# Kernel optimization log

Measured on AMD Instinct MI355X. Metric: run time of the kernel, lower is better.

## Reference

```python
import jax, jax.numpy as jnp
import numpy as np
from jax import lax

B, N, G, K, D = 16, 8192, 256, 64, 256
DEPTH, H, HID, PH = 4, 8, 1024, 128
EPS = 1e-5
BN_SCALE = float(1.0 / np.sqrt(1.0 + 1e-5))  # BatchNorm eval, running mean 0 / var 1


def setup_inputs() -> dict:
    key = jax.random.key(0)
    ks = iter(jax.random.split(key, 48))
    def rn(shape, s=0.02):
        return jax.random.normal(next(ks), shape, jnp.float32) * s
    z = lambda *s: jnp.zeros(s, jnp.float32)
    o = lambda *s: jnp.ones(s, jnp.float32)
    return dict(
        x=jax.random.normal(next(ks), (B, N, 3), jnp.float32),
        enc_w1=rn((3, 128)), enc_b1=z(128), enc_bn1_g=o(128), enc_bn1_b=z(128),
        enc_w2=rn((128, 256)), enc_b2=z(256),
        enc_w3=rn((512, 512)), enc_b3=z(512), enc_bn2_g=o(512), enc_bn2_b=z(512),
        enc_w4=rn((512, D)), enc_b4=z(D),
        cls_token=rn((1, 1, D)), cls_pos=rn((1, 1, D)),
        pos_w1=rn((3, 128)), pos_b1=z(128), pos_w2=rn((128, D)), pos_b2=z(D),
        ln1_g=o(DEPTH, D), ln1_b=z(DEPTH, D),
        qkv_w=rn((DEPTH, D, 3 * D)),
        proj_w=rn((DEPTH, D, D)), proj_b=z(DEPTH, D),
        ln2_g=o(DEPTH, D), ln2_b=z(DEPTH, D),
        fc1_w=rn((DEPTH, D, HID)), fc1_b=z(DEPTH, HID),
        fc2_w=rn((DEPTH, HID, D)), fc2_b=z(DEPTH, D),
        norm_g=o(D), norm_b=z(D),
        head_w1=rn((D + 3, PH)), head_b1=z(PH), head_w2=rn((PH, 1)), head_b2=z(1),
    )


def layernorm(t, g, b):
    m = jnp.mean(t, -1, keepdims=True)
    v = jnp.mean((t - m) ** 2, -1, keepdims=True)
    return (t - m) / jnp.sqrt(v + EPS) * g + b


def fps(xyz, num_group):
    # farthest point sampling; deterministic start at index 0 (torch uses randint)
    Bb, Nn, _ = xyz.shape
    def body(i, st):
        dist, far, idxs = st
        idxs = idxs.at[:, i].set(far)
        cen = jnp.take_along_axis(xyz, far[:, None, None], axis=1)  # (B,1,3)
        d = jnp.sum((xyz - cen) ** 2, -1)
        dist = jnp.minimum(dist, d)
        far = jnp.argmax(dist, axis=1).astype(jnp.int32)
        return (dist, far, idxs)
    st0 = (jnp.full((Bb, Nn), 1e10, jnp.float32),
           jnp.zeros((Bb,), jnp.int32),
           jnp.zeros((Bb, num_group), jnp.int32))
    _, _, idxs = lax.fori_loop(0, num_group, body, st0)
    centers = jnp.take_along_axis(xyz, idxs[..., None], axis=1)  # (B,G,3)
    return centers, idxs


def knn(xyz, centers, k):
    # squared-distance cdist (same argsort order as p=2) + topk smallest
    c2 = jnp.sum(centers ** 2, -1)[:, :, None]
    x2 = jnp.sum(xyz ** 2, -1)[:, None, :]
    d2 = c2 + x2 - 2.0 * jnp.einsum('bgd,bnd->bgn', centers, xyz)  # (B,G,N)
    idx = lax.top_k(-d2, k)[1]  # (B,G,k)
    neigh = jax.vmap(lambda p, i: p[i])(xyz, idx)  # (B,G,k,3)
    return idx, neigh


def _forward(x, enc_w1, enc_b1, enc_bn1_g, enc_bn1_b, enc_w2, enc_b2,
             enc_w3, enc_b3, enc_bn2_g, enc_bn2_b, enc_w4, enc_b4,
             cls_token, cls_pos, pos_w1, pos_b1, pos_w2, pos_b2,
             ln1_g, ln1_b, qkv_w, proj_w, proj_b, ln2_g, ln2_b,
             fc1_w, fc1_b, fc2_w, fc2_b, norm_g, norm_b,
             head_w1, head_b1, head_w2, head_b2):
    Bb, Nn, _ = x.shape
    # grouping is @torch.no_grad() in the original -> stop_gradient
    pts = lax.stop_gradient(x)
    centers, _ = fps(pts, G)
    idx, neigh = knn(pts, centers, K)
    neigh = neigh - centers[:, :, None, :]  # (B,G,K,3) centered

    # PointNet encoder (kernel-size-1 convs == matmuls; BN eval with unit stats)
    pg = neigh.reshape(Bb * G, K, 3)
    h = pg @ enc_w1 + enc_b1                                # (BG,K,128)
    h = jax.nn.relu(h * enc_bn1_g * BN_SCALE + enc_bn1_b)
    h = h @ enc_w2 + enc_b2                                 # (BG,K,256)
    gmax = jnp.max(h, axis=1, keepdims=True)                # (BG,1,256)
    h = jnp.concatenate([jnp.broadcast_to(gmax, h.shape), h], -1)  # (BG,K,512)
    h = h @ enc_w3 + enc_b3
    h = jax.nn.relu(h * enc_bn2_g * BN_SCALE + enc_bn2_b)
    h = h @ enc_w4 + enc_b4                                 # (BG,K,D)
    tokens = jnp.max(h, axis=1).reshape(Bb, G, D)

    pos = jax.nn.gelu(centers @ pos_w1 + pos_b1, approximate=False) @ pos_w2 + pos_b2
    xt = jnp.concatenate([jnp.broadcast_to(cls_token, (Bb, 1, D)), tokens], 1)
    pt = jnp.concatenate([jnp.broadcast_to(cls_pos, (Bb, 1, D)), pos], 1)

    scale = (D // H) ** -0.5
    for l in range(DEPTH):
        xi = xt + pt  # pos added before every block
        h1 = layernorm(xi, ln1_g[l], ln1_b[l])
        qkv = (h1 @ qkv_w[l]).reshape(Bb, G + 1, 3, H, D // H).transpose(2, 0, 3, 1, 4)
        q, k_, v = qkv[0], qkv[1], qkv[2]
        attn = jax.nn.softmax(jnp.einsum('bhnd,bhmd->bhnm', q, k_) * scale, -1)
        o = jnp.einsum('bhnm,bhmd->bhnd', attn, v).transpose(0, 2, 1, 3).reshape(Bb, G + 1, D)
        xi = xi + o @ proj_w[l] + proj_b[l]
        h2 = layernorm(xi, ln2_g[l], ln2_b[l])
        xi = xi + jax.nn.gelu(h2 @ fc1_w[l] + fc1_b[l], approximate=False) @ fc2_w[l] + fc2_b[l]
        xt = xi
    xt = layernorm(xt, norm_g, norm_b)

    gfeat = xt[:, 1:, :]  # (B,G,D)
    concat = jnp.concatenate(
        [jnp.broadcast_to(gfeat[:, :, None, :], (Bb, G, K, D)), neigh], -1)  # (B,G,K,D+3)
    lg = (jax.nn.relu(concat @ head_w1 + head_b1) @ head_w2 + head_b2)[..., 0]  # (B,G,K)

    # scatter-mean per-point logits over original N points
    flat_i = idx.reshape(Bb, G * K)
    flat_v = lg.reshape(Bb, G * K)
    sums = jax.vmap(lambda v, i: jax.ops.segment_sum(v, i, num_segments=N))(flat_v, flat_i)
    cnts = jax.vmap(lambda i: jax.ops.segment_sum(jnp.ones(i.shape, jnp.float32), i, num_segments=N))(flat_i)
    return sums / jnp.maximum(cnts, 1.0)  # (B,N)


def reference(x, enc_w1, enc_b1, enc_bn1_g, enc_bn1_b, enc_w2, enc_b2,
              enc_w3, enc_b3, enc_bn2_g, enc_bn2_b, enc_w4, enc_b4,
              cls_token, cls_pos, pos_w1, pos_b1, pos_w2, pos_b2,
              ln1_g, ln1_b, qkv_w, proj_w, proj_b, ln2_g, ln2_b,
              fc1_w, fc1_b, fc2_w, fc2_b, norm_g, norm_b,
              head_w1, head_b1, head_w2, head_b2):
    return _forward(x, enc_w1, enc_b1, enc_bn1_g, enc_bn1_b, enc_w2, enc_b2,
                    enc_w3, enc_b3, enc_bn2_g, enc_bn2_b, enc_w4, enc_b4,
                    cls_token, cls_pos, pos_w1, pos_b1, pos_w2, pos_b2,
                    ln1_g, ln1_b, qkv_w, proj_w, proj_b, ln2_g, ln2_b,
                    fc1_w, fc1_b, fc2_w, fc2_b, norm_g, norm_b,
                    head_w1, head_b1, head_w2, head_b2)
```

## Files before the change

kernel.cpp:

```cpp
#include <hip/hip_runtime.h>
#include <hip/hip_bf16.h>

#define B_ 16
#define N_ 8192
#define G_ 256
#define K_ 64
#define D_ 256
#define HID_ 1024
#define EPS_ 1e-5f

typedef __attribute__((ext_vector_type(8))) short bf16x8;
typedef __attribute__((ext_vector_type(4))) float f32x4;

__device__ __forceinline__ float bf16_to_f32(unsigned short u){
  unsigned int v = ((unsigned int)u) << 16;
  return __uint_as_float(v);
}
__device__ __forceinline__ unsigned short f32_to_bf16(float f){
  unsigned int u = __float_as_uint(f);
  unsigned int r = (u + 0x7FFFu + ((u >> 16) & 1u)) >> 16;
  return (unsigned short)r;
}
__device__ __forceinline__ unsigned short bf16h(float a){
  __hip_bfloat16 h = __float2bfloat16(a);
  union { __hip_bfloat16 h; unsigned short u; } cv; cv.h = h; return cv.u;
}
__device__ __forceinline__ float gelu_exact(float v){
  return 0.5f * v * (1.0f + erff(v * 0.70710678118654752440f));
}

template<int CTRL>
__device__ __forceinline__ unsigned long long dpp64(unsigned long long k){
  int lo = (int)(unsigned int)k;
  int hi = (int)(unsigned int)(k >> 32);
  int dlo = __builtin_amdgcn_update_dpp(lo, lo, CTRL, 0xF, 0xF, false);
  int dhi = __builtin_amdgcn_update_dpp(hi, hi, CTRL, 0xF, 0xF, false);
  return (((unsigned long long)(unsigned int)dhi) << 32) | (unsigned int)dlo;
}
__device__ __forceinline__ unsigned long long bcast64(unsigned long long k, int lane){
  unsigned int lo = (unsigned int)__builtin_amdgcn_readlane((int)(unsigned int)k, lane);
  unsigned int hi = (unsigned int)__builtin_amdgcn_readlane((int)(unsigned int)(k >> 32), lane);
  return (((unsigned long long)hi) << 32) | lo;
}
__device__ __forceinline__ unsigned long long wave_max64(unsigned long long k){
  unsigned long long t;
  t = dpp64<0x111>(k); if (t > k) k = t;
  t = dpp64<0x112>(k); if (t > k) k = t;
  t = dpp64<0x114>(k); if (t > k) k = t;
  t = dpp64<0x118>(k); if (t > k) k = t;
  t = dpp64<0x142>(k); if (t > k) k = t;
  t = dpp64<0x143>(k); if (t > k) k = t;
  return bcast64(k, 63);
}
__device__ __forceinline__ unsigned long long wave_min64(unsigned long long k){
  unsigned long long t;
  t = dpp64<0x111>(k); if (t < k) k = t;
  t = dpp64<0x112>(k); if (t < k) k = t;
  t = dpp64<0x114>(k); if (t < k) k = t;
  t = dpp64<0x118>(k); if (t < k) k = t;
  t = dpp64<0x142>(k); if (t < k) k = t;
  t = dpp64<0x143>(k); if (t < k) k = t;
  return bcast64(k, 63);
}
__device__ __forceinline__ unsigned long long red8_max64(unsigned long long k){
  unsigned long long t;
  t = dpp64<0x111>(k); if (t > k) k = t;
  t = dpp64<0x112>(k); if (t > k) k = t;
  t = dpp64<0x114>(k); if (t > k) k = t;
  return bcast64(k, 7);
}
__device__ __forceinline__ unsigned long long red4_min64(unsigned long long k){
  unsigned long long t;
  t = dpp64<0x111>(k); if (t < k) k = t;
  t = dpp64<0x112>(k); if (t < k) k = t;
  return bcast64(k, 3);
}

__device__ __forceinline__ void packHi(const float* __restrict__ W, unsigned short* __restrict__ hi,
                                       int f, int N, int ksBits){
  int j = f & 7, lane = (f >> 3) & 63;
  int ks = (f >> 9) & ((1 << ksBits) - 1);
  int nt = f >> (9 + ksBits);
  int k = ks * 32 + ((lane >> 4) & 3) * 8 + j, c = nt * 16 + (lane & 15);
  hi[f] = f32_to_bf16(W[(size_t)k * N + c]);
}

__global__ __launch_bounds__(512)
__attribute__((amdgpu_waves_per_eu(2, 2)))
void prep_fps_kernel(
    const float* __restrict__ x, float* __restrict__ centers,
    const float* __restrict__ w1, const float* __restrict__ b1,
    const float* __restrict__ g1, const float* __restrict__ bb1,
    const float* __restrict__ w3, const float* __restrict__ b3,
    const float* __restrict__ g2, const float* __restrict__ bb2,
    const float* __restrict__ enc_w2, const float* __restrict__ enc_w4,
    const float* __restrict__ qkv_w, const float* __restrict__ proj_w,
    const float* __restrict__ fc1_w, const float* __restrict__ fc2_w,
    float* __restrict__ w1f, float* __restrict__ b1f, float* __restrict__ b3f,
    unsigned short* __restrict__ w2ph, unsigned short* __restrict__ w2pl,
    unsigned short* __restrict__ w3ph, unsigned short* __restrict__ w4ph,
    unsigned short* __restrict__ qkvPh, unsigned short* __restrict__ projPh,
    unsigned short* __restrict__ fc1Ph, unsigned short* __restrict__ fc2Ph,
    unsigned short* __restrict__ w3tp)
{
  const float S = 0.99999500003749968f;
  int blk = blockIdx.x, tid = threadIdx.x;

  if (blk >= 17){
    int f = (blk - 17) * 512 + tid;
    if (f < 32768){
      int j = f & 7, lane = (f >> 3) & 63, ks = (f >> 9) & 3, nt = f >> 11;
      int k = ks * 32 + ((lane >> 4) & 3) * 8 + j, c = nt * 16 + (lane & 15);
      float v = enc_w2[(size_t)k * 256 + c];
      unsigned short h = f32_to_bf16(v);
      w2ph[f] = h; w2pl[f] = f32_to_bf16(v - bf16_to_f32(h));
    } else if (f < 163840){
      f -= 32768;
      int j = f & 7, lane = (f >> 3) & 63, ks = (f >> 9) & 7, nt = f >> 12;
      int k = ks * 32 + ((lane >> 4) & 3) * 8 + j, c = nt * 16 + (lane & 15);
      w3ph[f] = f32_to_bf16(w3[(size_t)(256 + k) * 512 + c] * g2[c] * S);
    } else if (f < 294912){
      f -= 163840;
      packHi(enc_w4, w4ph, f, 256, 4);
    } else if (f < 1081344){
      f -= 294912;
      int l = f / 196608, fl = f - l * 196608;
      packHi(qkv_w + (size_t)l * 196608, qkvPh + (size_t)l * 196608, fl, 768, 3);
    } else if (f < 1343488){
      f -= 1081344;
      int l = f >> 16, fl = f & 65535;
      packHi(proj_w + (size_t)l * 65536, projPh + (size_t)l * 65536, fl, 256, 3);
    } else if (f < 2392064){
      f -= 1343488;
      int l = f >> 18, fl = f & 262143;
      packHi(fc1_w + (size_t)l * 262144, fc1Ph + (size_t)l * 262144, fl, 1024, 3);
    } else if (f < 3440640){
      f -= 2392064;
      int l = f >> 18, fl = f & 262143;
      packHi(fc2_w + (size_t)l * 262144, fc2Ph + (size_t)l * 262144, fl, 256, 5);
    } else {
      f -= 3440640;
      int j = f & 7, lane = (f >> 3) & 63, ks = (f >> 9) & 7, nt = f >> 12;
      int k = ks * 32 + ((lane >> 4) & 3) * 8 + j, c = nt * 16 + (lane & 15);
      w3tp[f] = f32_to_bf16(w3[(size_t)k * 512 + c] * g2[c] * S);
    }
    return;
  }
  if (blk == 16){
    if (tid < 384) w1f[tid] = w1[tid] * g1[tid & 127] * S;
    if (tid < 128) b1f[tid] = b1[tid] * g1[tid] * S + bb1[tid];
    b3f[tid] = b3[tid] * g2[tid] * S + bb2[tid];
    return;
  }

  int b = blk;
  const float* xb = x + (size_t)b * N_ * 3;
  int lane = tid & 63, wave = tid >> 6;
  float px[16], py[16], pz[16], dist[16];
#pragma unroll
  for (int j = 0; j < 16; j++){
    int p = tid + j * 512;
    px[j] = xb[p*3+0]; py[j] = xb[p*3+1]; pz[j] = xb[p*3+2];
    dist[j] = 1e10f;
  }
#pragma unroll
  for (int j = 0; j < 16; j++)
    asm volatile("" : "+v"(px[j]), "+v"(py[j]), "+v"(pz[j]));

  __shared__ unsigned long long slotK[2][8];
  __shared__ float4 slotC[2][8];
  __shared__ float sCen[G_ * 3];
  float cx = xb[0], cy = xb[1], cz = xb[2];
  for (int i = 0; i < G_; i++){
    if (tid == 0){
      sCen[i*3+0] = cx; sCen[i*3+1] = cy; sCen[i*3+2] = cz;
    }
    float bestv = -1.0f; int bestj = 0;
#pragma unroll
    for (int j = 0; j < 16; j++){
      float dx = __fadd_rn(px[j], -cx);
      float dy = __fadd_rn(py[j], -cy);
      float dz = __fadd_rn(pz[j], -cz);
      float d  = __fadd_rn(__fadd_rn(__fmul_rn(dx,dx), __fmul_rn(dy,dy)), __fmul_rn(dz,dz));
      float dm = fminf(dist[j], d);
      dist[j] = dm;
      if (dm > bestv){ bestv = dm; bestj = j; }
    }
    unsigned int pid = (unsigned int)(tid + bestj * 512);
    unsigned long long key = (((unsigned long long)__float_as_uint(bestv)) << 32) | (unsigned long long)(~pid);
    key = wave_max64(key);
    int par = i & 1;
    unsigned int wpid = ~(unsigned int)key;
    if (lane == (int)(wpid & 63)){
      int jj = (int)(wpid >> 9);
      float fx = px[0], fy = py[0], fz = pz[0];
#pragma unroll
      for (int j = 1; j < 16; j++) if (jj == j){ fx = px[j]; fy = py[j]; fz = pz[j]; }
      slotK[par][wave] = key;
      slotC[par][wave] = make_float4(fx, fy, fz, 0.0f);
    }
    __syncthreads();
    if (i + 1 < G_){
      int sl = lane & 7;
      unsigned long long k2 = slotK[par][sl];
      float4 cc4 = slotC[par][sl];
      k2 = red8_max64(k2);
      unsigned int gpid = ~(unsigned int)k2;
      int s = (int)((gpid & 511u) >> 6);
      cx = __uint_as_float((unsigned int)__builtin_amdgcn_readlane((int)__float_as_uint(cc4.x), s));
      cy = __uint_as_float((unsigned int)__builtin_amdgcn_readlane((int)__float_as_uint(cc4.y), s));
      cz = __uint_as_float((unsigned int)__builtin_amdgcn_readlane((int)__float_as_uint(cc4.z), s));
    }
  }
  __syncthreads();
  for (int e = tid; e < G_ * 3; e += 512)
    centers[(size_t)b * G_ * 3 + e] = sCen[e];
}

__global__ __launch_bounds__(256)
__attribute__((amdgpu_waves_per_eu(4, 4)))
void knn_kernel(const float* __restrict__ x, const float* __restrict__ centers,
                int* __restrict__ knn_idx, float* __restrict__ neigh)
{
  int blk = blockIdx.x, b = blk >> 8;
  const float* xb = x + (size_t)b * N_ * 3;
  const float* cc = centers + (size_t)blk * 3;
  int tid = threadIdx.x, lane = tid & 63, wave = tid >> 6;
  float c0 = cc[0], c1 = cc[1], c2v = cc[2];
  float c2s = __fadd_rn(__fadd_rn(__fmul_rn(c0,c0), __fmul_rn(c1,c1)), __fmul_rn(c2v,c2v));
  float d[32];
#pragma unroll
  for (int j = 0; j < 32; j++){
    int p = tid + j * 256;
    float x0 = xb[p*3+0], x1 = xb[p*3+1], x2 = xb[p*3+2];
    float xs = __fadd_rn(__fadd_rn(__fmul_rn(x0,x0), __fmul_rn(x1,x1)), __fmul_rn(x2,x2));
    float dt = __fadd_rn(__fadd_rn(__fmul_rn(c0,x0), __fmul_rn(c1,x1)), __fmul_rn(c2v,x2));
    d[j] = __fadd_rn(__fadd_rn(c2s, xs), -__fmul_rn(2.0f, dt));
  }
#pragma unroll
  for (int j = 0; j < 32; j++) asm volatile("" : "+v"(d[j]));
  const float FINF = __int_as_float(0x7F800000);
  float lmin = FINF; unsigned int lp = 0xFFFFFFFFu;
#pragma unroll
  for (int j = 0; j < 32; j++){ if (d[j] < lmin){ lmin = d[j]; lp = (unsigned int)(tid + j*256); } }
  __shared__ unsigned long long wred[2][4];
  __shared__ int sIdx[K_];
  __shared__ float sNei[K_ * 3];
  for (int r = 0; r < K_; r++){
    unsigned int u = __float_as_uint(lmin);
    u = (u & 0x80000000u) ? ~u : (u | 0x80000000u);
    unsigned long long key = (((unsigned long long)u) << 32) | (unsigned long long)lp;
    key = wave_min64(key);
    int cur = r & 1;
    if (lane == 0) wred[cur][wave] = key;
    __syncthreads();
    unsigned long long m = red4_min64(wred[cur][lane & 3]);
    unsigned int p = (unsigned int)(m & 0xFFFFFFFFull);
    if (tid == (p & 255u)){
      sIdx[r] = (int)p;
      sNei[r*3+0] = __fadd_rn(xb[p*3+0], -c0);
      sNei[r*3+1] = __fadd_rn(xb[p*3+1], -c1);
      sNei[r*3+2] = __fadd_rn(xb[p*3+2], -c2v);
      lmin = FINF; lp = 0xFFFFFFFFu;
#pragma unroll
      for (int j = 0; j < 32; j++){
        if ((unsigned int)(tid + j*256) == p) d[j] = FINF;
        if (d[j] < lmin){ lmin = d[j]; lp = (unsigned int)(tid + j*256); }
      }
    }
  }
  __syncthreads();
  if (tid < K_) knn_idx[(size_t)blk * K_ + tid] = sIdx[tid];
  if (tid < K_ * 3) neigh[(size_t)blk * K_ * 3 + tid] = sNei[tid];
}

__global__ __launch_bounds__(256, 2) void encoder_kernel(
    const float* __restrict__ neigh,
    const float* __restrict__ w1f, const float* __restrict__ b1f,
    const unsigned short* __restrict__ w2ph, const unsigned short* __restrict__ w2pl,
    const float* __restrict__ b2,
    const float* __restrict__ b3f,
    const unsigned short* __restrict__ w3ph, const unsigned short* __restrict__ w3tp,
    const unsigned short* __restrict__ w4ph,
    const float* __restrict__ b4,
    float* __restrict__ tokens)
{
  __shared__ __align__(16) unsigned short sH1[64 * 136];
  __shared__ __align__(16) unsigned short sH2[64 * 264];
  __shared__ __align__(16) float sShared[256];
  float (*sNeigh)[4] = (float(*)[4])sShared;
  unsigned short* sGmaxBf = (unsigned short*)sShared;

  int tid  = threadIdx.x;
  int wave = tid >> 6, lane = tid & 63, quad = lane >> 4, lrow = lane & 15;
  size_t gid = blockIdx.x;

  if (tid < 192) sNeigh[tid / 3][tid % 3] = neigh[gid * 192 + tid];
  __syncthreads();

  for (int e = tid; e < 8192; e += 256){
    int r = e >> 7, c = e & 127;
    float v = fmaf(sNeigh[r][2], w1f[256 + c], fmaf(sNeigh[r][1], w1f[128 + c], fmaf(sNeigh[r][0], w1f[c], b1f[c])));
    sH1[r * 136 + c] = bf16h(fmaxf(v, 0.0f));
  }
  __syncthreads();

  {
    f32x4 acc[4][4];
    const f32x4 z = {0.f, 0.f, 0.f, 0.f};
#pragma unroll
    for (int mt = 0; mt < 4; mt++)
#pragma unroll
      for (int nl = 0; nl < 4; nl++) acc[mt][nl] = z;
#pragma unroll
    for (int ks = 0; ks < 4; ks++){
      bf16x8 af[4];
#pragma unroll
      for (int mt = 0; mt < 4; mt++)
        af[mt] = *(const bf16x8*)&sH1[(mt*16 + lrow)*136 + ks*32 + quad*8];
#pragma unroll
      for (int nl = 0; nl < 4; nl++){
        size_t bo = (((size_t)(wave*4 + nl)*4 + ks)*64 + lane)*8;
        bf16x8 bh = *(const bf16x8*)&w2ph[bo];
        bf16x8 bl = *(const bf16x8*)&w2pl[bo];
#pragma unroll
        for (int mt = 0; mt < 4; mt++){
          acc[mt][nl] = __builtin_amdgcn_mfma_f32_16x16x32_bf16(af[mt], bh, acc[mt][nl], 0, 0, 0);
          acc[mt][nl] = __builtin_amdgcn_mfma_f32_16x16x32_bf16(af[mt], bl, acc[mt][nl], 0, 0, 0);
        }
      }
    }
#pragma unroll
    for (int nl = 0; nl < 4; nl++){
      int col = wave*64 + nl*16 + lrow;
      float bias = b2[col];
#pragma unroll
      for (int mt = 0; mt < 4; mt++)
#pragma unroll
        for (int rg = 0; rg < 4; rg++)
          sH2[(mt*16 + quad*4 + rg)*264 + col] = bf16h(acc[mt][nl][rg] + bias);
    }
  }
  __syncthreads();

  {
    float mx = -3.4e38f;
#pragma unroll 8
    for (int r = 0; r < 64; r++) mx = fmaxf(mx, bf16_to_f32(sH2[r*264 + tid]));
    sGmaxBf[tid] = bf16h(mx);
  }
  __syncthreads();

  f32x4 acc4[4][4];
  {
    const f32x4 z = {0.f, 0.f, 0.f, 0.f};
#pragma unroll
    for (int mt = 0; mt < 4; mt++)
#pragma unroll
      for (int nl = 0; nl < 4; nl++) acc4[mt][nl] = z;
  }
  for (int cc = 0; cc < 4; cc++){
    f32x4 acc3[4][2], accg[2];
    {
      const f32x4 z = {0.f, 0.f, 0.f, 0.f};
#pragma unroll
      for (int mt = 0; mt < 4; mt++){ acc3[mt][0] = z; acc3[mt][1] = z; }
      accg[0] = z; accg[1] = z;
    }
#pragma unroll
    for (int ks = 0; ks < 8; ks++){
      bf16x8 gf = *(const bf16x8*)&sGmaxBf[ks*32 + quad*8];
#pragma unroll
      for (int nl = 0; nl < 2; nl++){
        int nt = cc*8 + wave*2 + nl;
        size_t bo = (((size_t)nt*8 + ks)*64 + lane)*8;
        bf16x8 bh = *(const bf16x8*)&w3tp[bo];
        accg[nl] = __builtin_amdgcn_mfma_f32_16x16x32_bf16(gf, bh, accg[nl], 0, 0, 0);
      }
    }
#pragma unroll
    for (int ks = 0; ks < 8; ks++){
      bf16x8 af[4];
#pragma unroll
      for (int mt = 0; mt < 4; mt++)
        af[mt] = *(const bf16x8*)&sH2[(mt*16 + lrow)*264 + ks*32 + quad*8];
#pragma unroll
      for (int nl = 0; nl < 2; nl++){
        int nt = cc*8 + wave*2 + nl;
        size_t bo = (((size_t)nt*8 + ks)*64 + lane)*8;
        bf16x8 bh = *(const bf16x8*)&w3ph[bo];
#pragma unroll
        for (int mt = 0; mt < 4; mt++)
          acc3[mt][nl] = __builtin_amdgcn_mfma_f32_16x16x32_bf16(af[mt], bh, acc3[mt][nl], 0, 0, 0);
      }
    }
    __syncthreads();
#pragma unroll
    for (int nl = 0; nl < 2; nl++){
      int cl = wave*32 + nl*16 + lrow;
      int c  = cc*128 + cl;
      float bb = b3f[c];
#pragma unroll
      for (int mt = 0; mt < 4; mt++)
#pragma unroll
        for (int rg = 0; rg < 4; rg++)
          sH1[(mt*16 + quad*4 + rg)*136 + cl] = bf16h(fmaxf(acc3[mt][nl][rg] + accg[nl][rg] + bb, 0.0f));
    }
    __syncthreads();
#pragma unroll
    for (int ks = 0; ks < 4; ks++){
      bf16x8 af[4];
#pragma unroll
      for (int mt = 0; mt < 4; mt++)
        af[mt] = *(const bf16x8*)&sH1[(mt*16 + lrow)*136 + ks*32 + quad*8];
#pragma unroll
      for (int nl = 0; nl < 4; nl++){
        int nt = wave*4 + nl;
        size_t bo = (((size_t)nt*16 + cc*4 + ks)*64 + lane)*8;
        bf16x8 bh = *(const bf16x8*)&w4ph[bo];
#pragma unroll
        for (int mt = 0; mt < 4; mt++)
          acc4[mt][nl] = __builtin_amdgcn_mfma_f32_16x16x32_bf16(af[mt], bh, acc4[mt][nl], 0, 0, 0);
      }
    }
  }

#pragma unroll
  for (int nl = 0; nl < 4; nl++){
    float mx = -3.4e38f;
#pragma unroll
    for (int mt = 0; mt < 4; mt++)
#pragma unroll
      for (int rg = 0; rg < 4; rg++) mx = fmaxf(mx, acc4[mt][nl][rg]);
    mx = fmaxf(mx, __shfl_xor(mx, 16));
    mx = fmaxf(mx, __shfl_xor(mx, 32));
    if (quad == 0){
      int col = wave*64 + nl*16 + lrow;
      tokens[gid * 256 + col] = mx + b4[col];
    }
  }
}

__global__ __launch_bounds__(128) void pos_ln_kernel(
    const float* __restrict__ centers, const float* __restrict__ tokens,
    const float* __restrict__ cls_token, const float* __restrict__ cls_pos,
    const float* __restrict__ pw1, const float* __restrict__ pb1,
    const float* __restrict__ pw2, const float* __restrict__ pb2,
    const float* __restrict__ lng, const float* __restrict__ lnb,
    float* __restrict__ pt, float* __restrict__ xi, unsigned short* __restrict__ lnbuf)
{
  __shared__ float hS[128];
  __shared__ float red[2][2];
  int row = blockIdx.x;
  int b = row / 257, n = row - b * 257;
  int tid = threadIdx.x;
  size_t ro = (size_t)row * 256;
  float u0, u1;
  if (n == 0){
    float p0 = cls_pos[tid], p1 = cls_pos[128 + tid];
    u0 = cls_token[tid] + p0; u1 = cls_token[128 + tid] + p1;
    pt[ro + tid] = p0; pt[ro + 128 + tid] = p1;
  } else {
    int g = n - 1;
    const float* c = centers + ((size_t)b * 256 + g) * 3;
    float h = fmaf(c[2], pw1[256 + tid], fmaf(c[1], pw1[128 + tid], fmaf(c[0], pw1[tid], pb1[tid])));
    hS[tid] = gelu_exact(h);
    __syncthreads();
    const float* tok = tokens + ((size_t)b * 256 + g) * 256;
    float s0 = pb2[tid], s1 = pb2[128 + tid];
#pragma unroll 4
    for (int k = 0; k < 128; k++){
      s0 = fmaf(hS[k], pw2[(size_t)k * 256 + tid], s0);
      s1 = fmaf(hS[k], pw2[(size_t)k * 256 + 128 + tid], s1);
    }
    pt[ro + tid] = s0; pt[ro + 128 + tid] = s1;
    u0 = tok[tid] + s0; u1 = tok[128 + tid] + s1;
  }
  float s = u0 + u1, q = u0*u0 + u1*u1;
#pragma unroll
  for (int o = 32; o; o >>= 1){ s += __shfl_down(s, o); q += __shfl_down(q, o); }
  int wv = tid >> 6;
  if ((tid & 63) == 0){ red[0][wv] = s; red[1][wv] = q; }
  __syncthreads();
  float m  = (red[0][0] + red[0][1]) * (1.0f / 256.0f);
  float var = (red[1][0] + red[1][1]) * (1.0f / 256.0f) - m * m;
  float rs = 1.0f / sqrtf(var + EPS_);
  xi[ro + tid] = u0; xi[ro + 128 + tid] = u1;
  lnbuf[ro + tid] = bf16h((u0 - m) * rs * lng[tid] + lnb[tid]);
  lnbuf[ro + 128 + tid] = bf16h((u1 - m) * rs * lng[128 + tid] + lnb[128 + tid]);
}

template<int ACT>
__global__ __launch_bounds__(256, 2) void mfma_gemm(
    const unsigned short* __restrict__ A, const unsigned short* __restrict__ Bh,
    const float* __restrict__ bias, unsigned short* __restrict__ C, int M, int K, int N)
{
  __shared__ __align__(16) unsigned short sA[32 * 72];
  int tid = threadIdx.x;
  int wave = tid >> 6, lane = tid & 63, quad = lane >> 4, lrow = lane & 15;
  int row0 = blockIdx.x * 32;
  int col0 = blockIdx.y * 128;
  int ksTotal = K >> 5;
  f32x4 acc[2][2];
  const f32x4 z = {0.f, 0.f, 0.f, 0.f};
#pragma unroll
  for (int mt = 0; mt < 2; mt++){ acc[mt][0] = z; acc[mt][1] = z; }

  for (int k0 = 0; k0 < K; k0 += 64){
    {
      int r = tid >> 3, c8 = (tid & 7) * 8;
      int gr = row0 + r;
      bf16x8 v = {0,0,0,0,0,0,0,0};
      if (gr < M) v = *(const bf16x8*)(A + (size_t)gr * K + k0 + c8);
      *(bf16x8*)&sA[r * 72 + c8] = v;
    }
    __syncthreads();
    int ksBase = k0 >> 5;
#pragma unroll
    for (int ks = 0; ks < 2; ks++){
      bf16x8 af[2];
#pragma unroll
      for (int mt = 0; mt < 2; mt++)
        af[mt] = *(const bf16x8*)&sA[(mt*16 + lrow)*72 + ks*32 + quad*8];
#pragma unroll
      for (int nl = 0; nl < 2; nl++){
        int nt = (col0 >> 4) + wave*2 + nl;
        size_t bo = (((size_t)nt * ksTotal + ksBase + ks)*64 + lane)*8;
        bf16x8 bh = *(const bf16x8*)&Bh[bo];
#pragma unroll
        for (int mt = 0; mt < 2; mt++)
          acc[mt][nl] = __builtin_amdgcn_mfma_f32_16x16x32_bf16(af[mt], bh, acc[mt][nl], 0, 0, 0);
      }
    }
    __syncthreads();
  }
#pragma unroll
  for (int nl = 0; nl < 2; nl++){
    int c = col0 + wave*32 + nl*16 + lrow;
    float bc = bias ? bias[c] : 0.0f;
#pragma unroll
    for (int mt = 0; mt < 2; mt++)
#pragma unroll
      for (int rg = 0; rg < 4; rg++){
        int r = row0 + mt*16 + quad*4 + rg;
        if (r < M){
          float v = acc[mt][nl][rg] + bc;
          if (ACT == 1) v = gelu_exact(v);
          C[(size_t)r * N + c] = bf16h(v);
        }
      }
  }
}

__global__ __launch_bounds__(256, 2) void mfma_gemm_ln(
    const unsigned short* __restrict__ A, const unsigned short* __restrict__ Bh,
    const float* __restrict__ bias, const float* __restrict__ res,
    const float* __restrict__ ptb,
    float* __restrict__ C, float* __restrict__ xiOut, unsigned short* __restrict__ lnOut,
    const float* __restrict__ lng, const float* __restrict__ lnb, int M, int K)
{
  __shared__ __align__(16) unsigned short sA[16 * 72];
  __shared__ float sRed[2][16][4];
  int tid = threadIdx.x;
  int wave = tid >> 6, lane = tid & 63, quad = lane >> 4, lrow = lane & 15;
  int row0 = blockIdx.x * 16;
  int ksTotal = K >> 5;
  f32x4 acc[4];
  const f32x4 z = {0.f, 0.f, 0.f, 0.f};
#pragma unroll
  for (int nl = 0; nl < 4; nl++) acc[nl] = z;

  for (int k0 = 0; k0 < K; k0 += 64){
    if (tid < 128){
      int r = tid >> 3, c8 = (tid & 7) * 8;
      int gr = row0 + r;
      bf16x8 v = {0,0,0,0,0,0,0,0};
      if (gr < M) v = *(const bf16x8*)(A + (size_t)gr * K + k0 + c8);
      *(bf16x8*)&sA[r * 72 + c8] = v;
    }
    __syncthreads();
    int ksBase = k0 >> 5;
#pragma unroll
    for (int ks = 0; ks < 2; ks++){
      bf16x8 af = *(const bf16x8*)&sA[lrow*72 + ks*32 + quad*8];
#pragma unroll
      for (int nl = 0; nl < 4; nl++){
        int nt = wave*4 + nl;
        size_t bo = (((size_t)nt * ksTotal + ksBase + ks)*64 + lane)*8;
        bf16x8 bh = *(const bf16x8*)&Bh[bo];
        acc[nl] = __builtin_amdgcn_mfma_f32_16x16x32_bf16(af, bh, acc[nl], 0, 0, 0);
      }
    }
    __syncthreads();
  }
#pragma unroll
  for (int nl = 0; nl < 4; nl++){
    int c = wave*64 + nl*16 + lrow;
    float bc = bias[c];
#pragma unroll
    for (int rg = 0; rg < 4; rg++){
      int r = row0 + quad*4 + rg;
      if (r < M){
        float v = acc[nl][rg] + bc + res[(size_t)r * 256 + c];
        if (C) C[(size_t)r * 256 + c] = v;
        float u = v;
        if (ptb) u += ptb[(size_t)r * 256 + c];
        acc[nl][rg] = u;
      }
    }
  }
#pragma unroll
  for (int rg = 0; rg < 4; rg++){
    int rloc = quad*4 + rg;
    float s = 0.0f, q = 0.0f;
#pragma unroll
    for (int nl = 0; nl < 4; nl++){ float u = acc[nl][rg]; s += u; q += u*u; }
#pragma unroll
    for (int off = 1; off < 16; off <<= 1){ s += __shfl_xor(s, off); q += __shfl_xor(q, off); }
    if (lrow == 0){ sRed[0][rloc][wave] = s; sRed[1][rloc][wave] = q; }
  }
  __syncthreads();
#pragma unroll
  for (int rg = 0; rg < 4; rg++){
    int rloc = quad*4 + rg;
    int r = row0 + rloc;
    if (r >= M) continue;
    float s = ((sRed[0][rloc][0] + sRed[0][rloc][1]) + sRed[0][rloc][2]) + sRed[0][rloc][3];
    float q = ((sRed[1][rloc][0] + sRed[1][rloc][1]) + sRed[1][rloc][2]) + sRed[1][rloc][3];
    float m  = s * (1.0f / 256.0f);
    float var = q * (1.0f / 256.0f) - m * m;
    float rs = 1.0f / sqrtf(var + EPS_);
#pragma unroll
    for (int nl = 0; nl < 4; nl++){
      int c = wave*64 + nl*16 + lrow;
      float u = acc[nl][rg];
      lnOut[(size_t)r * 256 + c] = bf16h((u - m) * rs * lng[c] + lnb[c]);
      if (xiOut) xiOut[(size_t)r * 256 + c] = u;
    }
  }
}

__global__ __launch_bounds__(256, 2) void mlp_fused(
    const unsigned short* __restrict__ A,
    const unsigned short* __restrict__ B1,
    const float* __restrict__ bias1,
    const unsigned short* __restrict__ B2,
    const float* __restrict__ bias2,
    const float* __restrict__ res,
    const float* __restrict__ ptb,
    float* __restrict__ xiOut, unsigned short* __restrict__ lnOut,
    const float* __restrict__ lng, const float* __restrict__ lnb, int M)
{
  __shared__ __align__(16) unsigned short sA[16 * 264];
  __shared__ __align__(16) unsigned short sH[16 * 1032];
  __shared__ float sRed[2][16][4];
  int tid = threadIdx.x;
  int wave = tid >> 6, lane = tid & 63, quad = lane >> 4, lrow = lane & 15;
  int row0 = blockIdx.x * 16;

  for (int e = tid; e < 512; e += 256){
    int r = e >> 5, c8 = (e & 31) * 8;
    int gr = row0 + r;
    bf16x8 v = {0,0,0,0,0,0,0,0};
    if (gr < M) v = *(const bf16x8*)(A + (size_t)gr * 256 + c8);
    *(bf16x8*)&sA[r * 264 + c8] = v;
  }
  __syncthreads();

  {
    f32x4 acc1[16];
    const f32x4 z = {0.f, 0.f, 0.f, 0.f};
#pragma unroll
    for (int nl = 0; nl < 16; nl++) acc1[nl] = z;
#pragma unroll
    for (int ks = 0; ks < 8; ks++){
      bf16x8 af = *(const bf16x8*)&sA[lrow*264 + ks*32 + quad*8];
#pragma unroll
      for (int nl = 0; nl < 16; nl++){
        int nt = wave*16 + nl;
        size_t bo = (((size_t)nt*8 + ks)*64 + lane)*8;
        bf16x8 bh = *(const bf16x8*)&B1[bo];
        acc1[nl] = __builtin_amdgcn_mfma_f32_16x16x32_bf16(af, bh, acc1[nl], 0, 0, 0);
      }
    }
#pragma unroll
    for (int nl = 0; nl < 16; nl++){
      int c = wave*256 + nl*16 + lrow;
      float bc = bias1[c];
#pragma unroll
      for (int rg = 0; rg < 4; rg++)
        sH[(quad*4+rg)*1032 + c] = bf16h(gelu_exact(acc1[nl][rg] + bc));
    }
  }
  __syncthreads();

  f32x4 acc[4];
  const f32x4 z = {0.f, 0.f, 0.f, 0.f};
#pragma unroll
  for (int nl = 0; nl < 4; nl++) acc[nl] = z;
#pragma unroll 4
  for (int ks = 0; ks < 32; ks++){
    bf16x8 af = *(const bf16x8*)&sH[lrow*1032 + ks*32 + quad*8];
#pragma unroll
    for (int nl = 0; nl < 4; nl++){
      int nt = wave*4 + nl;
      size_t bo = (((size_t)nt*32 + ks)*64 + lane)*8;
      bf16x8 bh = *(const bf16x8*)&B2[bo];
      acc[nl] = __builtin_amdgcn_mfma_f32_16x16x32_bf16(af, bh, acc[nl], 0, 0, 0);
    }
  }
#pragma unroll
  for (int nl = 0; nl < 4; nl++){
    int c = wave*64 + nl*16 + lrow;
    float bc = bias2[c];
#pragma unroll
    for (int rg = 0; rg < 4; rg++){
      int r = row0 + quad*4 + rg;
      if (r < M){
        float v = acc[nl][rg] + bc + res[(size_t)r * 256 + c];
        float u = v;
        if (ptb) u += ptb[(size_t)r * 256 + c];
        acc[nl][rg] = u;
      }
    }
  }
#pragma unroll
  for (int rg = 0; rg < 4; rg++){
    int rloc = quad*4 + rg;
    float s = 0.0f, q = 0.0f;
#pragma unroll
    for (int nl = 0; nl < 4; nl++){ float u = acc[nl][rg]; s += u; q += u*u; }
#pragma unroll
    for (int off = 1; off < 16; off <<= 1){ s += __shfl_xor(s, off); q += __shfl_xor(q, off); }
    if (lrow == 0){ sRed[0][rloc][wave] = s; sRed[1][rloc][wave] = q; }
  }
  __syncthreads();
#pragma unroll
  for (int rg = 0; rg < 4; rg++){
    int rloc = quad*4 + rg;
    int r = row0 + rloc;
    if (r >= M) continue;
    float s = ((sRed[0][rloc][0] + sRed[0][rloc][1]) + sRed[0][rloc][2]) + sRed[0][rloc][3];
    float q = ((sRed[1][rloc][0] + sRed[1][rloc][1]) + sRed[1][rloc][2]) + sRed[1][rloc][3];
    float m  = s * (1.0f / 256.0f);
    float var = q * (1.0f / 256.0f) - m * m;
    float rs = 1.0f / sqrtf(var + EPS_);
#pragma unroll
    for (int nl = 0; nl < 4; nl++){
      int c = wave*64 + nl*16 + lrow;
      float u = acc[nl][rg];
      lnOut[(size_t)r * 256 + c] = bf16h((u - m) * rs * lng[c] + lnb[c]);
      if (xiOut) xiOut[(size_t)r * 256 + c] = u;
    }
  }
}

__global__ __launch_bounds__(256)
__attribute__((amdgpu_waves_per_eu(2, 4)))
void attn_kernel(const unsigned short* __restrict__ qkv, unsigned short* __restrict__ obuf)
{
  int bh = blockIdx.x;
  int b = bh >> 3, h = bh & 7;
  int tid = threadIdx.x;
  int qi = tid >> 2, kp = tid & 3;
  int qrow = blockIdx.y * 64 + qi;
  bool act = qrow < 257;
  __shared__ float kS[128][33];
  __shared__ float vS[128][33];
  const unsigned short* qb = qkv + (size_t)b * 257 * 768;
  float q[32], o[32];
  float mrun = -3.4e38f, l = 0.0f;
  if (act){
    const unsigned short* qr = qb + (size_t)qrow * 768 + h * 32;
#pragma unroll
    for (int j = 0; j < 32; j++){ q[j] = bf16_to_f32(qr[j]); o[j] = 0.0f; }
  } else {
#pragma unroll
    for (int j = 0; j < 32; j++){ q[j] = 0.0f; o[j] = 0.0f; }
  }
  const float scale = 0.17677669529663687f;
  for (int m0 = 0; m0 < 257; m0 += 128){
    int cnt = min(128, 257 - m0);
    for (int e = tid; e < cnt * 32; e += 256){
      int mm = e >> 5, j = e & 31;
      const unsigned short* rowp = qb + (size_t)(m0 + mm) * 768 + h * 32;
      kS[mm][j] = bf16_to_f32(rowp[256 + j]);
      vS[mm][j] = bf16_to_f32(rowp[512 + j]);
    }
    __syncthreads();
    if (act){
      for (int mm = kp; mm < cnt; mm += 4){
        float s = 0.0f;
#pragma unroll
        for (int j = 0; j < 32; j++) s = fmaf(q[j], kS[mm][j], s);
        s *= scale;
        float nm = fmaxf(mrun, s);
        float alpha = expf(mrun - nm);
        float p = expf(s - nm);
        l = fmaf(l, alpha, p);
#pragma unroll
        for (int j = 0; j < 32; j++) o[j] = fmaf(p, vS[mm][j], o[j] * alpha);
        mrun = nm;
      }
    }
    __syncthreads();
  }
  if (act){
#pragma unroll
    for (int msk = 1; msk <= 2; msk <<= 1){
      float m2 = __shfl_xor(mrun, msk);
      float l2 = __shfl_xor(l, msk);
      float nm = fmaxf(mrun, m2);
      float a1 = expf(mrun - nm), a2 = expf(m2 - nm);
      l = l * a1 + l2 * a2;
#pragma unroll
      for (int j = 0; j < 32; j++){
        float o2 = __shfl_xor(o[j], msk);
        o[j] = o[j] * a1 + o2 * a2;
      }
      mrun = nm;
    }
    if (kp == 0){
      float inv = 1.0f / l;
      unsigned short* orow = obuf + (size_t)(b * 257 + qrow) * 256 + h * 32;
#pragma unroll
      for (int j = 0; j < 32; j++) orow[j] = bf16h(o[j] * inv);
    }
  }
}

__global__ __launch_bounds__(256) void head_kernel(
    const unsigned short* __restrict__ gfeat, const float* __restrict__ neigh, const int* __restrict__ knn_idx,
    const float* __restrict__ w1, const float* __restrict__ b1,
    const float* __restrict__ w2, const float* __restrict__ b2,
    float* __restrict__ sums, float* __restrict__ cnts)
{
  int blk = blockIdx.x, b = blk >> 8;
  __shared__ float xS[256];
  __shared__ float nS[64][4];
  __shared__ float partH[2][128];
  __shared__ float sharedH[128];
  __shared__ float w2S[128];
  __shared__ float wtail[3][128];
  int tid = threadIdx.x;
  xS[tid] = bf16_to_f32(gfeat[((size_t)b * 257 + 1 + (blk & 255)) * 256 + tid]);
  if (tid < 192) nS[tid / 3][tid % 3] = neigh[(size_t)blk * 192 + tid];
  if (tid < 128){
    w2S[tid] = w2[tid];
    wtail[0][tid] = w1[256 * 128 + tid];
    wtail[1][tid] = w1[257 * 128 + tid];
    wtail[2][tid] = w1[258 * 128 + tid];
  }
  __syncthreads();
  {
    int half = tid >> 7, j = tid & 127;
    float s = 0.0f;
#pragma unroll 8
    for (int k = 0; k < 128; k++) s = fmaf(xS[half * 128 + k], w1[(size_t)(half * 128 + k) * 128 + j], s);
    partH[half][j] = s;
  }
  __syncthreads();
  if (tid < 128) sharedH[tid] = partH[0][tid] + partH[1][tid] + b1[tid];
  __syncthreads();
  int r = tid >> 2, q = tid & 3;
  float n0 = nS[r][0], n1 = nS[r][1], n2 = nS[r][2];
  float s = 0.0f;
#pragma unroll
  for (int j0 = 0; j0 < 32; j0++){
    int j = q * 32 + j0;
    float h = fmaf(n2, wtail[2][j], fmaf(n1, wtail[1][j], fmaf(n0, wtail[0][j], sharedH[j])));
    s = fmaf(fmaxf(h, 0.0f), w2S[j], s);
  }
  s += __shfl_xor(s, 1);
  s += __shfl_xor(s, 2);
  if (q == 0){
    float lg = s + b2[0];
    int p = knn_idx[(size_t)blk * K_ + r];
    atomicAdd(&sums[(size_t)b * N_ + p], lg);
    atomicAdd(&cnts[(size_t)b * N_ + p], 1.0f);
  }
}

__global__ void finalize_kernel(const float* __restrict__ sums, const float* __restrict__ cnts, float* __restrict__ out)
{
  int i = blockIdx.x * 256 + threadIdx.x;
  out[i] = sums[i] / fmaxf(cnts[i], 1.0f);
}

extern "C" void kernel_launch(void* const* d_in, const int* in_sizes, int n_in,
                              void* d_out, int out_size, void* d_ws, size_t ws_size,
                              hipStream_t stream)
{
  (void)in_sizes; (void)n_in; (void)out_size; (void)ws_size;
  const float* x        = (const float*)d_in[0];
  const float* enc_w1   = (const float*)d_in[1];
  const float* enc_b1   = (const float*)d_in[2];
  const float* enc_bn1g = (const float*)d_in[3];
  const float* enc_bn1b = (const float*)d_in[4];
  const float* enc_w2   = (const float*)d_in[5];
  const float* enc_b2   = (const float*)d_in[6];
  const float* enc_w3   = (const float*)d_in[7];
  const float* enc_b3   = (const float*)d_in[8];
  const float* enc_bn2g = (const float*)d_in[9];
  const float* enc_bn2b = (const float*)d_in[10];
  const float* enc_w4   = (const float*)d_in[11];
  const float* enc_b4   = (const float*)d_in[12];
  const float* cls_tok  = (const float*)d_in[13];
  const float* cls_pos  = (const float*)d_in[14];
  const float* pos_w1   = (const float*)d_in[15];
  const float* pos_b1   = (const float*)d_in[16];
  const float* pos_w2   = (const float*)d_in[17];
  const float* pos_b2   = (const float*)d_in[18];
  const float* ln1_g    = (const float*)d_in[19];
  const float* ln1_b    = (const float*)d_in[20];
  const float* qkv_w    = (const float*)d_in[21];
  const float* proj_w   = (const float*)d_in[22];
  const float* proj_b   = (const float*)d_in[23];
  const float* ln2_g    = (const float*)d_in[24];
  const float* ln2_b    = (const float*)d_in[25];
  const float* fc1_w    = (const float*)d_in[26];
  const float* fc1_b    = (const float*)d_in[27];
  const float* fc2_w    = (const float*)d_in[28];
  const float* fc2_b    = (const float*)d_in[29];
  const float* norm_g   = (const float*)d_in[30];
  const float* norm_b   = (const float*)d_in[31];
  const float* head_w1  = (const float*)d_in[32];
  const float* head_b1  = (const float*)d_in[33];
  const float* head_w2  = (const float*)d_in[34];
  const float* head_b2  = (const float*)d_in[35];

  float* ws = (float*)d_ws;
  size_t off = 0;
  auto alloc = [&](size_t n)->float*{ float* p = ws + off; off += (n + 63) & ~(size_t)63; return p; };

  float* centers = alloc((size_t)B_ * G_ * 3);
  float* w1f     = alloc(384);
  float* b1f     = alloc(128);
  float* b3f     = alloc(512);
  unsigned short* w2ph = (unsigned short*)alloc(16384);
  unsigned short* w2pl = (unsigned short*)alloc(16384);
  unsigned short* w3ph = (unsigned short*)alloc(65536);
  unsigned short* w3tp = (unsigned short*)alloc(65536);
  unsigned short* w4ph = (unsigned short*)alloc(65536);
  unsigned short* qkvPh = (unsigned short*)alloc(393216);
  unsigned short* projPh = (unsigned short*)alloc(131072);
  unsigned short* fc1Ph = (unsigned short*)alloc(524288);
  unsigned short* fc2Ph = (unsigned short*)alloc(524288);
  float* tokens  = alloc((size_t)B_ * G_ * D_);
  float* neigh   = alloc((size_t)B_ * G_ * K_ * 3);
  int*   knn_idx = (int*)alloc((size_t)B_ * G_ * K_);
  float* pt      = alloc((size_t)B_ * 257 * D_);
  float* xi      = alloc((size_t)B_ * 257 * D_);
  unsigned short* lnbufB = (unsigned short*)alloc((size_t)B_ * 257 * D_ / 2 + 64);
  unsigned short* obufB  = (unsigned short*)alloc((size_t)B_ * 257 * D_ / 2 + 64);
  unsigned short* bigbufB= (unsigned short*)alloc((size_t)B_ * 257 * HID_ / 2 + 64);
  unsigned short* gfeatB = (unsigned short*)alloc((size_t)B_ * 257 * D_ / 2 + 64);
  float* sums    = alloc((size_t)B_ * N_);
  float* cnts    = alloc((size_t)B_ * N_);

  hipMemsetAsync(sums, 0, (size_t)2 * B_ * N_ * sizeof(float), stream);

  prep_fps_kernel<<<6993, 512, 0, stream>>>(x, centers,
      enc_w1, enc_b1, enc_bn1g, enc_bn1b, enc_w3, enc_b3, enc_bn2g, enc_bn2b,
      enc_w2, enc_w4, qkv_w, proj_w, fc1_w, fc2_w,
      w1f, b1f, b3f, w2ph, w2pl, w3ph, w4ph, qkvPh, projPh, fc1Ph, fc2Ph, w3tp);

  knn_kernel<<<B_ * G_, 256, 0, stream>>>(x, centers, knn_idx, neigh);
  encoder_kernel<<<B_ * G_, 256, 0, stream>>>(neigh, w1f, b1f, w2ph, w2pl, enc_b2,
                                              b3f, w3ph, w3tp, w4ph, enc_b4, tokens);
  pos_ln_kernel<<<B_ * 257, 128, 0, stream>>>(centers, tokens, cls_tok, cls_pos,
                                              pos_w1, pos_b1, pos_w2, pos_b2,
                                              ln1_g, ln1_b, pt, xi, lnbufB);
  const int M = B_ * 257;
  for (int l = 0; l < 4; l++){
    mfma_gemm<0><<<dim3(129, 6), 256, 0, stream>>>(lnbufB, qkvPh + (size_t)l*196608, nullptr, bigbufB, M, 256, 768);
    attn_kernel<<<dim3(B_ * 8, 5), 256, 0, stream>>>(bigbufB, obufB);
    mfma_gemm_ln<<<257, 256, 0, stream>>>(obufB, projPh + (size_t)l*65536, proj_b + l*256, xi, nullptr,
                                          xi, nullptr, lnbufB, ln2_g + l*256, ln2_b + l*256, M, 256);
    if (l < 3){
      mlp_fused<<<257, 256, 0, stream>>>(lnbufB, fc1Ph + (size_t)l*262144, fc1_b + l*1024,
                                         fc2Ph + (size_t)l*262144, fc2_b + l*256, xi, pt,
                                         xi, lnbufB, ln1_g + (l+1)*256, ln1_b + (l+1)*256, M);
    } else {
      mlp_fused<<<257, 256, 0, stream>>>(lnbufB, fc1Ph + (size_t)l*262144, fc1_b + l*1024,
                                         fc2Ph + (size_t)l*262144, fc2_b + l*256, xi, nullptr,
                                         nullptr, gfeatB, norm_g, norm_b, M);
    }
  }
  head_kernel<<<B_ * G_, 256, 0, stream>>>(gfeatB, neigh, knn_idx, head_w1, head_b1, head_w2, head_b2, sums, cnts);
  finalize_kernel<<<(B_ * N_) / 256, 256, 0, stream>>>(sums, cnts, (float*)d_out);
}
```

Baseline: 1.594 ms.

## Fuse KNN into FPS kernel with per-batch progress flags to overlap stages

KNN work moves into the prep/FPS launch as extra blocks. The FPS blocks now publish centers directly to global memory and release a per-batch progress counter every four iterations. KNN blocks spin on that counter and start grouping as soon as their center exists, so KNN overlaps the long serial FPS loop and one kernel launch is removed. KNN blocks also change from 256 to 512 threads with 16 points per thread and an 8-way cross-wave reduction. The risk is a deadlock if spinning KNN blocks are scheduled before the FPS blocks and fill the GPU, which depends on block dispatch order; the spinning also uses up CU slots.

```diff
diff --git a/kernel.cpp b/kernel.cpp
--- a/kernel.cpp
+++ b/kernel.cpp
@@ -69,11 +69,12 @@
   t = dpp64<0x114>(k); if (t > k) k = t;
   return bcast64(k, 7);
 }
-__device__ __forceinline__ unsigned long long red4_min64(unsigned long long k){
+__device__ __forceinline__ unsigned long long red8_min64(unsigned long long k){
   unsigned long long t;
   t = dpp64<0x111>(k); if (t < k) k = t;
   t = dpp64<0x112>(k); if (t < k) k = t;
-  return bcast64(k, 3);
+  t = dpp64<0x114>(k); if (t < k) k = t;
+  return bcast64(k, 7);
 }
 
 __device__ __forceinline__ void packHi(const float* __restrict__ W, unsigned short* __restrict__ hi,
@@ -89,6 +90,8 @@
 __attribute__((amdgpu_waves_per_eu(2, 2)))
 void prep_fps_kernel(
     const float* __restrict__ x, float* __restrict__ centers,
+    int* __restrict__ prog,
+    int* __restrict__ knn_idx, float* __restrict__ neigh,
     const float* __restrict__ w1, const float* __restrict__ b1,
     const float* __restrict__ g1, const float* __restrict__ bb1,
     const float* __restrict__ w3, const float* __restrict__ b3,
@@ -106,7 +109,7 @@
   const float S = 0.99999500003749968f;
   int blk = blockIdx.x, tid = threadIdx.x;
 
-  if (blk >= 17){
+  if (blk >= 17 && blk < 6993){
     int f = (blk - 17) * 512 + tid;
     if (f < 32768){
       int j = f & 7, lane = (f >> 3) & 63, ks = (f >> 9) & 3, nt = f >> 11;
@@ -153,125 +156,128 @@
     return;
   }
 
-  int b = blk;
-  const float* xb = x + (size_t)b * N_ * 3;
-  int lane = tid & 63, wave = tid >> 6;
-  float px[16], py[16], pz[16], dist[16];
-#pragma unroll
-  for (int j = 0; j < 16; j++){
-    int p = tid + j * 512;
-    px[j] = xb[p*3+0]; py[j] = xb[p*3+1]; pz[j] = xb[p*3+2];
-    dist[j] = 1e10f;
-  }
-#pragma unroll
-  for (int j = 0; j < 16; j++)
-    asm volatile("" : "+v"(px[j]), "+v"(py[j]), "+v"(pz[j]));
-
-  __shared__ unsigned long long slotK[2][8];
-  __shared__ float4 slotC[2][8];
-  __shared__ float sCen[G_ * 3];
-  float cx = xb[0], cy = xb[1], cz = xb[2];
-  for (int i = 0; i < G_; i++){
+  if (blk < 16){
+    int b = blk;
+    const float* xb = x + (size_t)b * N_ * 3;
+    int lane = tid & 63, wave = tid >> 6;
+    float px[16], py[16], pz[16], dist[16];
+#pragma unroll
+    for (int j = 0; j < 16; j++){
+      int p = tid + j * 512;
+      px[j] = xb[p*3+0]; py[j] = xb[p*3+1]; pz[j] = xb[p*3+2];
+      dist[j] = 1e10f;
+    }
+#pragma unroll
+    for (int j = 0; j < 16; j++)
+      asm volatile("" : "+v"(px[j]), "+v"(py[j]), "+v"(pz[j]));
+
+    __shared__ unsigned long long slotK[2][8];
+    __shared__ float4 slotC[2][8];
+    float cx = xb[0], cy = xb[1], cz = xb[2];
+    for (int i = 0; i < G_; i++){
+      if (tid == 0){
+        float* cp = centers + ((size_t)b * G_ + i) * 3;
+        cp[0] = cx; cp[1] = cy; cp[2] = cz;
+        if ((i & 3) == 3 || i == G_ - 1)
+          __hip_atomic_store(&prog[b], i + 1, __ATOMIC_RELEASE, __HIP_MEMORY_SCOPE_AGENT);
+      }
+      float bestv = -1.0f; int bestj = 0;
+#pragma unroll
+      for (int j = 0; j < 16; j++){
+        float dx = __fadd_rn(px[j], -cx);
+        float dy = __fadd_rn(py[j], -cy);
+        float dz = __fadd_rn(pz[j], -cz);
+        float d  = __fadd_rn(__fadd_rn(__fmul_rn(dx,dx), __fmul_rn(dy,dy)), __fmul_rn(dz,dz));
+        float dm = fminf(dist[j], d);
+        dist[j] = dm;
+        if (dm > bestv){ bestv = dm; bestj = j; }
+      }
+      unsigned int pid = (unsigned int)(tid + bestj * 512);
+      unsigned long long key = (((unsigned long long)__float_as_uint(bestv)) << 32) | (unsigned long long)(~pid);
+      key = wave_max64(key);
+      int par = i & 1;
+      unsigned int wpid = ~(unsigned int)key;
+      if (lane == (int)(wpid & 63)){
+        int jj = (int)(wpid >> 9);
+        float fx = px[0], fy = py[0], fz = pz[0];
+#pragma unroll
+        for (int j = 1; j < 16; j++) if (jj == j){ fx = px[j]; fy = py[j]; fz = pz[j]; }
+        slotK[par][wave] = key;
+        slotC[par][wave] = make_float4(fx, fy, fz, 0.0f);
+      }
+      __syncthreads();
+      if (i + 1 < G_){
+        int sl = lane & 7;
+        unsigned long long k2 = slotK[par][sl];
+        float4 cc4 = slotC[par][sl];
+        k2 = red8_max64(k2);
+        unsigned int gpid = ~(unsigned int)k2;
+        int s = (int)((gpid & 511u) >> 6);
+        cx = __uint_as_float((unsigned int)__builtin_amdgcn_readlane((int)__float_as_uint(cc4.x), s));
+        cy = __uint_as_float((unsigned int)__builtin_amdgcn_readlane((int)__float_as_uint(cc4.y), s));
+        cz = __uint_as_float((unsigned int)__builtin_amdgcn_readlane((int)__float_as_uint(cc4.z), s));
+      }
+    }
+    return;
+  }
+
+  {
+    int kb = blk - 6993;
+    int b = kb >> 8, g = kb & 255;
+    __shared__ unsigned long long wred[2][8];
+    __shared__ int sIdx[K_];
+    __shared__ float sNei[K_ * 3];
     if (tid == 0){
-      sCen[i*3+0] = cx; sCen[i*3+1] = cy; sCen[i*3+2] = cz;
-    }
-    float bestv = -1.0f; int bestj = 0;
+      while (__hip_atomic_load(&prog[b], __ATOMIC_ACQUIRE, __HIP_MEMORY_SCOPE_AGENT) < g + 1)
+        __builtin_amdgcn_s_sleep(8);
+    }
+    __syncthreads();
+    const float* xb = x + (size_t)b * N_ * 3;
+    const float* cc = centers + ((size_t)b * G_ + g) * 3;
+    int lane = tid & 63, wave = tid >> 6;
+    float c0 = cc[0], c1 = cc[1], c2v = cc[2];
+    float c2s = __fadd_rn(__fadd_rn(__fmul_rn(c0,c0), __fmul_rn(c1,c1)), __fmul_rn(c2v,c2v));
+    float d[16];
 #pragma unroll
     for (int j = 0; j < 16; j++){
-      float dx = __fadd_rn(px[j], -cx);
-      float dy = __fadd_rn(py[j], -cy);
-      float dz = __fadd_rn(pz[j], -cz);
-      float d  = __fadd_rn(__fadd_rn(__fmul_rn(dx,dx), __fmul_rn(dy,dy)), __fmul_rn(dz,dz));
-      float dm = fminf(dist[j], d);
-      dist[j] = dm;
-      if (dm > bestv){ bestv = dm; bestj = j; }
-    }
-    unsigned int pid = (unsigned int)(tid + bestj * 512);
-    unsigned long long key = (((unsigned long long)__float_as_uint(bestv)) << 32) | (unsigned long long)(~pid);
-    key = wave_max64(key);
-    int par = i & 1;
-    unsigned int wpid = ~(unsigned int)key;
-    if (lane == (int)(wpid & 63)){
-      int jj = (int)(wpid >> 9);
-      float fx = px[0], fy = py[0], fz = pz[0];
-#pragma unroll
-      for (int j = 1; j < 16; j++) if (jj == j){ fx = px[j]; fy = py[j]; fz = pz[j]; }
-      slotK[par][wave] = key;
-      slotC[par][wave] = make_float4(fx, fy, fz, 0.0f);
-    }
-    __syncthreads();
-    if (i + 1 < G_){
-      int sl = lane & 7;
-      unsigned long long k2 = slotK[par][sl];
-      float4 cc4 = slotC[par][sl];
-      k2 = red8_max64(k2);
-      unsigned int gpid = ~(unsigned int)k2;
-      int s = (int)((gpid & 511u) >> 6);
-      cx = __uint_as_float((unsigned int)__builtin_amdgcn_readlane((int)__float_as_uint(cc4.x), s));
-      cy = __uint_as_float((unsigned int)__builtin_amdgcn_readlane((int)__float_as_uint(cc4.y), s));
-      cz = __uint_as_float((unsigned int)__builtin_amdgcn_readlane((int)__float_as_uint(cc4.z), s));
-    }
-  }
-  __syncthreads();
-  for (int e = tid; e < G_ * 3; e += 512)
-    centers[(size_t)b * G_ * 3 + e] = sCen[e];
-}
-
-__global__ __launch_bounds__(256)
-__attribute__((amdgpu_waves_per_eu(4, 4)))
-void knn_kernel(const float* __restrict__ x, const float* __restrict__ centers,
-                int* __restrict__ knn_idx, float* __restrict__ neigh)
-{
-  int blk = blockIdx.x, b = blk >> 8;
-  const float* xb = x + (size_t)b * N_ * 3;
-  const float* cc = centers + (size_t)blk * 3;
-  int tid = threadIdx.x, lane = tid & 63, wave = tid >> 6;
-  float c0 = cc[0], c1 = cc[1], c2v = cc[2];
-  float c2s = __fadd_rn(__fadd_rn(__fmul_rn(c0,c0), __fmul_rn(c1,c1)), __fmul_rn(c2v,c2v));
-  float d[32];
-#pragma unroll
-  for (int j = 0; j < 32; j++){
-    int p = tid + j * 256;
-    float x0 = xb[p*3+0], x1 = xb[p*3+1], x2 = xb[p*3+2];
-    float xs = __fadd_rn(__fadd_rn(__fmul_rn(x0,x0), __fmul_rn(x1,x1)), __fmul_rn(x2,x2));
-    float dt = __fadd_rn(__fadd_rn(__fmul_rn(c0,x0), __fmul_rn(c1,x1)), __fmul_rn(c2v,x2));
-    d[j] = __fadd_rn(__fadd_rn(c2s, xs), -__fmul_rn(2.0f, dt));
-  }
-#pragma unroll
-  for (int j = 0; j < 32; j++) asm volatile("" : "+v"(d[j]));
-  const float FINF = __int_as_float(0x7F800000);
-  float lmin = FINF; unsigned int lp = 0xFFFFFFFFu;
-#pragma unroll
-  for (int j = 0; j < 32; j++){ if (d[j] < lmin){ lmin = d[j]; lp = (unsigned int)(tid + j*256); } }
-  __shared__ unsigned long long wred[2][4];
-  __shared__ int sIdx[K_];
-  __shared__ float sNei[K_ * 3];
-  for (int r = 0; r < K_; r++){
-    unsigned int u = __float_as_uint(lmin);
-    u = (u & 0x80000000u) ? ~u : (u | 0x80000000u);
-    unsigned long long key = (((unsigned long long)u) << 32) | (unsigned long long)lp;
-    key = wave_min64(key);
-    int cur = r & 1;
-    if (lane == 0) wred[cur][wave] = key;
-    __syncthreads();
-    unsigned long long m = red4_min64(wred[cur][lane & 3]);
-    unsigned int p = (unsigned int)(m & 0xFFFFFFFFull);
-    if (tid == (p & 255u)){
-      sIdx[r] = (int)p;
-      sNei[r*3+0] = __fadd_rn(xb[p*3+0], -c0);
-      sNei[r*3+1] = __fadd_rn(xb[p*3+1], -c1);
-      sNei[r*3+2] = __fadd_rn(xb[p*3+2], -c2v);
-      lmin = FINF; lp = 0xFFFFFFFFu;
-#pragma unroll
-      for (int j = 0; j < 32; j++){
-        if ((unsigned int)(tid + j*256) == p) d[j] = FINF;
-        if (d[j] < lmin){ lmin = d[j]; lp = (unsigned int)(tid + j*256); }
-      }
-    }
-  }
-  __syncthreads();
-  if (tid < K_) knn_idx[(size_t)blk * K_ + tid] = sIdx[tid];
-  if (tid < K_ * 3) neigh[(size_t)blk * K_ * 3 + tid] = sNei[tid];
+      int p = tid + j * 512;
+      float x0 = xb[p*3+0], x1 = xb[p*3+1], x2 = xb[p*3+2];
+      float xs = __fadd_rn(__fadd_rn(__fmul_rn(x0,x0), __fmul_rn(x1,x1)), __fmul_rn(x2,x2));
+      float dt = __fadd_rn(__fadd_rn(__fmul_rn(c0,x0), __fmul_rn(c1,x1)), __fmul_rn(c2v,x2));
+      d[j] = __fadd_rn(__fadd_rn(c2s, xs), -__fmul_rn(2.0f, dt));
+    }
+    const float FINF = __int_as_float(0x7F800000);
+    float lmin = FINF; unsigned int lp = 0xFFFFFFFFu;
+#pragma unroll
+    for (int j = 0; j < 16; j++){ if (d[j] < lmin){ lmin = d[j]; lp = (unsigned int)(tid + j*512); } }
+    for (int r = 0; r < K_; r++){
+      unsigned int u = __float_as_uint(lmin);
+      u = (u & 0x80000000u) ? ~u : (u | 0x80000000u);
+      unsigned long long key = (((unsigned long long)u) << 32) | (unsigned long long)lp;
+      key = wave_min64(key);
+      int cur = r & 1;
+      if (lane == 0) wred[cur][wave] = key;
+      __syncthreads();
+      unsigned long long m = red8_min64(wred[cur][lane & 7]);
+      unsigned int p = (unsigned int)(m & 0xFFFFFFFFull);
+      if (tid == (int)(p & 511u)){
+        sIdx[r] = (int)p;
+        sNei[r*3+0] = __fadd_rn(xb[p*3+0], -c0);
+        sNei[r*3+1] = __fadd_rn(xb[p*3+1], -c1);
+        sNei[r*3+2] = __fadd_rn(xb[p*3+2], -c2v);
+        lmin = FINF; lp = 0xFFFFFFFFu;
+#pragma unroll
+        for (int j = 0; j < 16; j++){
+          if ((unsigned int)(tid + j*512) == p) d[j] = FINF;
+          if (d[j] < lmin){ lmin = d[j]; lp = (unsigned int)(tid + j*512); }
+        }
+      }
+    }
+    __syncthreads();
+    size_t gblk = (size_t)b * G_ + g;
+    if (tid < K_) knn_idx[gblk * K_ + tid] = sIdx[tid];
+    if (tid < K_ * 3) neigh[gblk * K_ * 3 + tid] = sNei[tid];
+  }
 }
 
 __global__ __launch_bounds__(256, 2) void encoder_kernel(
@@ -955,17 +961,17 @@
   unsigned short* obufB  = (unsigned short*)alloc((size_t)B_ * 257 * D_ / 2 + 64);
   unsigned short* bigbufB= (unsigned short*)alloc((size_t)B_ * 257 * HID_ / 2 + 64);
   unsigned short* gfeatB = (unsigned short*)alloc((size_t)B_ * 257 * D_ / 2 + 64);
+  int*   prog    = (int*)alloc(64);
   float* sums    = alloc((size_t)B_ * N_);
   float* cnts    = alloc((size_t)B_ * N_);
 
-  hipMemsetAsync(sums, 0, (size_t)2 * B_ * N_ * sizeof(float), stream);
-
-  prep_fps_kernel<<<6993, 512, 0, stream>>>(x, centers,
+  hipMemsetAsync(prog, 0, (64 + (size_t)2 * B_ * N_) * sizeof(float), stream);
+
+  prep_fps_kernel<<<11089, 512, 0, stream>>>(x, centers, prog, knn_idx, neigh,
       enc_w1, enc_b1, enc_bn1g, enc_bn1b, enc_w3, enc_b3, enc_bn2g, enc_bn2b,
       enc_w2, enc_w4, qkv_w, proj_w, fc1_w, fc2_w,
       w1f, b1f, b3f, w2ph, w2pl, w3ph, w4ph, qkvPh, projPh, fc1Ph, fc2Ph, w3tp);
 
-  knn_kernel<<<B_ * G_, 256, 0, stream>>>(x, centers, knn_idx, neigh);
   encoder_kernel<<<B_ * G_, 256, 0, stream>>>(neigh, w1f, b1f, w2ph, w2pl, enc_b2,
                                               b3f, w3ph, w3tp, w4ph, enc_b4, tokens);
   pos_ln_kernel<<<B_ * 257, 128, 0, stream>>>(centers, tokens, cls_tok, cls_pos,
```

Result: slower. 1.992 ms (+25.0%).
